# Kernel optimization log

Measured on AMD Instinct MI355X. Metric: run time of the kernel, lower is better.

Reference implementation:

```python
import jax, jax.numpy as jnp
import numpy as np

C = 1.0  # Poincare ball curvature
EPS = 1e-15


def setup_inputs() -> dict:
    key = jax.random.key(0)
    k1, k2, k3 = jax.random.split(key, 3)
    B, S, D_IN, D_OUT = 16, 8192, 128, 128
    # points strictly inside the unit ball: ||x|| ~ 0.05*sqrt(128) ~ 0.57
    x = 0.05 * jax.random.normal(k1, (B, S, D_IN), dtype=jnp.float32)
    z = 0.01 * jax.random.normal(k2, (D_IN, D_OUT), dtype=jnp.float32)  # init_std=0.01 normal
    r = 0.01 * jax.random.normal(k3, (D_OUT,), dtype=jnp.float32)
    return {"x": x, "z": z, "r": r}


def reference(x, z, r):
    # Poincare MLR (Shimizu et al., Hyperbolic NN++), as in hypll PoincareBall.mlr
    c = jnp.asarray(C, x.dtype)
    cs = jnp.sqrt(c)
    prefix = x.shape[:-1]
    x2 = x.reshape(-1, x.shape[-1])                       # [N, d_in]
    # conformal factor lambda_x = 2 / (1 - c ||x||^2)
    lam = 2.0 / (1.0 - c * jnp.sum(x2 * x2, axis=-1, keepdims=True))  # [N, 1]
    z_norm = jnp.maximum(jnp.linalg.norm(z, axis=0), EPS)             # [d_out]
    two_csr = 2.0 * cs * r                                            # [d_out]
    inner = x2 @ z                                                    # [N, d_out]
    arg = (cs * lam * inner / z_norm) * jnp.cosh(two_csr) - (lam - 1.0) * jnp.sinh(two_csr)
    out = (2.0 * z_norm / cs) * jnp.arcsinh(arg)                      # [N, d_out]
    return out.reshape(*prefix, z.shape[1])
```

## Files before the change

kernel.cpp:

```cpp
#include <hip/hip_runtime.h>
#include <cstdint>


typedef __attribute__((ext_vector_type(8))) short short8;
typedef __attribute__((ext_vector_type(4))) float floatx4;

#define D 128
#define ZT_STRIDE 136
#define TILE_M 128

__device__ inline unsigned bf16_rne(float f) {
    unsigned u = __float_as_uint(f);
    return ((u + 0x7FFFu + ((u >> 16) & 1u)) >> 16) & 0xFFFFu;
}

__global__ void hmlr_prep(const float* __restrict__ z, const float* __restrict__ r,
                          unsigned short* __restrict__ zt, float* __restrict__ An,
                          float* __restrict__ Bn, float* __restrict__ Sn) {
    int n = blockIdx.x;
    int k = threadIdx.x;
    float v = z[k * D + n];
    zt[n * ZT_STRIDE + k] = (unsigned short)bf16_rne(v);
    float p = v * v;
    #pragma unroll
    for (int off = 32; off >= 1; off >>= 1) p += __shfl_down(p, off, 64);
    __shared__ float tmp[2];
    if ((k & 63) == 0) tmp[k >> 6] = p;
    __syncthreads();
    if (k == 0) {
        float ss = tmp[0] + tmp[1];
        float zn = fmaxf(sqrtf(ss), 1e-15f);
        float tc = 2.0f * r[n];
        An[n] = coshf(tc) / zn;
        Bn[n] = sinhf(tc);
        Sn[n] = 2.0f * zn;
    }
}

__global__ __launch_bounds__(256) void hmlr_main(const float* __restrict__ x,
                                                 const unsigned short* __restrict__ zt,
                                                 const float* __restrict__ An,
                                                 const float* __restrict__ Bn,
                                                 const float* __restrict__ Sn,
                                                 float* __restrict__ out) {
    __shared__ __align__(16) unsigned short Xlds[TILE_M * ZT_STRIDE];
    __shared__ float rowss[TILE_M];

    const int t    = threadIdx.x;
    const int w    = t >> 6;
    const int l    = t & 63;
    const int quad = l >> 4;
    const int l15  = l & 15;

    const int row0 = blockIdx.x * TILE_M;
    const float4* xv = reinterpret_cast<const float4*>(x) + (size_t)blockIdx.x * (TILE_M * D / 4);

    #pragma unroll
    for (int i = 0; i < 16; ++i) {
        int f4  = t + 256 * i;
        float4 v = xv[f4];
        int row = f4 >> 5;
        int k4  = (f4 & 31) << 2;
        float ssq = v.x * v.x + v.y * v.y + v.z * v.z + v.w * v.w;
        ssq += __shfl_xor(ssq, 1);
        ssq += __shfl_xor(ssq, 2);
        ssq += __shfl_xor(ssq, 4);
        ssq += __shfl_xor(ssq, 8);
        ssq += __shfl_xor(ssq, 16);
        if ((t & 31) == 0) rowss[row] = ssq;
        unsigned lo = bf16_rne(v.x) | (bf16_rne(v.y) << 16);
        unsigned hi = bf16_rne(v.z) | (bf16_rne(v.w) << 16);
        *reinterpret_cast<uint2*>(&Xlds[row * ZT_STRIDE + k4]) = make_uint2(lo, hi);
    }
    __syncthreads();

    floatx4 acc[2][8];
    #pragma unroll
    for (int mt = 0; mt < 2; ++mt)
        #pragma unroll
        for (int nt = 0; nt < 8; ++nt)
            acc[mt][nt] = (floatx4){0.f, 0.f, 0.f, 0.f};

    #pragma unroll
    for (int kc = 0; kc < 4; ++kc) {
        const int kof = kc * 32 + quad * 8;
        short8 a0 = *reinterpret_cast<const short8*>(&Xlds[(w * 32 + l15) * ZT_STRIDE + kof]);
        short8 a1 = *reinterpret_cast<const short8*>(&Xlds[(w * 32 + 16 + l15) * ZT_STRIDE + kof]);
        #pragma unroll
        for (int nt = 0; nt < 8; ++nt) {
            short8 b = *reinterpret_cast<const short8*>(zt + (nt * 16 + l15) * ZT_STRIDE + kof);
            acc[0][nt] = __builtin_amdgcn_mfma_f32_16x16x32_bf16(a0, b, acc[0][nt], 0, 0, 0);
            acc[1][nt] = __builtin_amdgcn_mfma_f32_16x16x32_bf16(a1, b, acc[1][nt], 0, 0, 0);
        }
    }

    float anv[8], bnv[8], snv[8];
    #pragma unroll
    for (int nt = 0; nt < 8; ++nt) {
        int n = nt * 16 + l15;
        anv[nt] = An[n];
        bnv[nt] = Bn[n];
        snv[nt] = Sn[n];
    }
    #pragma unroll
    for (int mt = 0; mt < 2; ++mt) {
        #pragma unroll
        for (int reg = 0; reg < 4; ++reg) {
            int rlocal = w * 32 + mt * 16 + quad * 4 + reg;
            float lam  = 2.0f / (1.0f - rowss[rlocal]);
            float lm1  = lam - 1.0f;
            float* orow = out + (size_t)(row0 + rlocal) * D + l15;
            #pragma unroll
            for (int nt = 0; nt < 8; ++nt) {
                float inner = acc[mt][nt][reg];
                float arg = __fmaf_rn(lam * inner, anv[nt], -lm1 * bnv[nt]);
                float a  = fabsf(arg);
                float as = __logf(a + __fsqrt_rn(__fmaf_rn(a, a, 1.0f)));
                orow[nt * 16] = copysignf(as, arg) * snv[nt];
            }
        }
    }
}

extern "C" void kernel_launch(void* const* d_in, const int* in_sizes, int n_in,
                              void* d_out, int out_size, void* d_ws, size_t ws_size,
                              hipStream_t stream) {
    const float* x = (const float*)d_in[0];
    const float* z = (const float*)d_in[1];
    const float* r = (const float*)d_in[2];
    float* out = (float*)d_out;

    char* wsb = (char*)d_ws;
    unsigned short* zt = (unsigned short*)wsb;
    float* An = (float*)(wsb + 128 * ZT_STRIDE * sizeof(unsigned short));
    float* Bn = An + 128;
    float* Sn = An + 256;

    hmlr_prep<<<128, 128, 0, stream>>>(z, r, zt, An, Bn, Sn);

    const int n_rows = in_sizes[0] / D;
    hmlr_main<<<n_rows / TILE_M, 256, 0, stream>>>(x, zt, An, Bn, Sn, out);
}
```

Before: 147.8 us.

## Load x directly into MFMA A-fragments in registers, dropping LDS staging

Each lane now loads its own row's fp32 slice of x straight from global memory in the layout the MFMA A operand expects, converts it to bf16 in registers, and computes the row norm with cross-lane shuffles. This removes the LDS tile, the barrier and the LDS round trip. Block tile size drops to 64 rows, with each wave handling 16 rows, so there are twice as many blocks. The trade-off is less coalesced global loads (32-byte chunks per lane spread across rows) and a zt B-fragment reload per 16 rows instead of per 32.

Measured after the change: 140.3 us. 5.1% less time.

```diff
diff --git a/kernel.cpp b/kernel.cpp
--- a/kernel.cpp
+++ b/kernel.cpp
@@ -7,7 +7,6 @@
 
 #define D 128
 #define ZT_STRIDE 136
-#define TILE_M 128
 
 __device__ inline unsigned bf16_rne(float f) {
     unsigned u = __float_as_uint(f);
@@ -43,54 +42,57 @@
                                                  const float* __restrict__ Bn,
                                                  const float* __restrict__ Sn,
                                                  float* __restrict__ out) {
-    __shared__ __align__(16) unsigned short Xlds[TILE_M * ZT_STRIDE];
-    __shared__ float rowss[TILE_M];
-
     const int t    = threadIdx.x;
     const int w    = t >> 6;
     const int l    = t & 63;
     const int quad = l >> 4;
     const int l15  = l & 15;
 
-    const int row0 = blockIdx.x * TILE_M;
-    const float4* xv = reinterpret_cast<const float4*>(x) + (size_t)blockIdx.x * (TILE_M * D / 4);
+    const int rowbase = blockIdx.x * 64 + w * 16;
+    const int myrow   = rowbase + l15;
 
+    const float* xrow = x + (size_t)myrow * D + quad * 8;
+    float4 xv[8];
     #pragma unroll
-    for (int i = 0; i < 16; ++i) {
-        int f4  = t + 256 * i;
-        float4 v = xv[f4];
-        int row = f4 >> 5;
-        int k4  = (f4 & 31) << 2;
-        float ssq = v.x * v.x + v.y * v.y + v.z * v.z + v.w * v.w;
-        ssq += __shfl_xor(ssq, 1);
-        ssq += __shfl_xor(ssq, 2);
-        ssq += __shfl_xor(ssq, 4);
-        ssq += __shfl_xor(ssq, 8);
-        ssq += __shfl_xor(ssq, 16);
-        if ((t & 31) == 0) rowss[row] = ssq;
-        unsigned lo = bf16_rne(v.x) | (bf16_rne(v.y) << 16);
-        unsigned hi = bf16_rne(v.z) | (bf16_rne(v.w) << 16);
-        *reinterpret_cast<uint2*>(&Xlds[row * ZT_STRIDE + k4]) = make_uint2(lo, hi);
+    for (int kc = 0; kc < 4; ++kc) {
+        xv[2 * kc]     = *reinterpret_cast<const float4*>(xrow + kc * 32);
+        xv[2 * kc + 1] = *reinterpret_cast<const float4*>(xrow + kc * 32 + 4);
     }
-    __syncthreads();
 
-    floatx4 acc[2][8];
+    float ssq = 0.f;
     #pragma unroll
-    for (int mt = 0; mt < 2; ++mt)
-        #pragma unroll
-        for (int nt = 0; nt < 8; ++nt)
-            acc[mt][nt] = (floatx4){0.f, 0.f, 0.f, 0.f};
+    for (int i = 0; i < 8; ++i)
+        ssq += xv[i].x * xv[i].x + xv[i].y * xv[i].y + xv[i].z * xv[i].z + xv[i].w * xv[i].w;
+    ssq += __shfl_xor(ssq, 16);
+    ssq += __shfl_xor(ssq, 32);
+
+    short8 afrag[4];
+    #pragma unroll
+    for (int kc = 0; kc < 4; ++kc) {
+        float4 v0 = xv[2 * kc], v1 = xv[2 * kc + 1];
+        union { short8 s8; unsigned short u[8]; } af;
+        af.u[0] = (unsigned short)bf16_rne(v0.x);
+        af.u[1] = (unsigned short)bf16_rne(v0.y);
+        af.u[2] = (unsigned short)bf16_rne(v0.z);
+        af.u[3] = (unsigned short)bf16_rne(v0.w);
+        af.u[4] = (unsigned short)bf16_rne(v1.x);
+        af.u[5] = (unsigned short)bf16_rne(v1.y);
+        af.u[6] = (unsigned short)bf16_rne(v1.z);
+        af.u[7] = (unsigned short)bf16_rne(v1.w);
+        afrag[kc] = af.s8;
+    }
+
+    floatx4 acc[8];
+    #pragma unroll
+    for (int nt = 0; nt < 8; ++nt) acc[nt] = (floatx4){0.f, 0.f, 0.f, 0.f};
 
     #pragma unroll
     for (int kc = 0; kc < 4; ++kc) {
-        const int kof = kc * 32 + quad * 8;
-        short8 a0 = *reinterpret_cast<const short8*>(&Xlds[(w * 32 + l15) * ZT_STRIDE + kof]);
-        short8 a1 = *reinterpret_cast<const short8*>(&Xlds[(w * 32 + 16 + l15) * ZT_STRIDE + kof]);
+        const unsigned short* zb = zt + kc * 32 + quad * 8;
         #pragma unroll
         for (int nt = 0; nt < 8; ++nt) {
-            short8 b = *reinterpret_cast<const short8*>(zt + (nt * 16 + l15) * ZT_STRIDE + kof);
-            acc[0][nt] = __builtin_amdgcn_mfma_f32_16x16x32_bf16(a0, b, acc[0][nt], 0, 0, 0);
-            acc[1][nt] = __builtin_amdgcn_mfma_f32_16x16x32_bf16(a1, b, acc[1][nt], 0, 0, 0);
+            short8 b = *reinterpret_cast<const short8*>(zb + (nt * 16 + l15) * ZT_STRIDE);
+            acc[nt] = __builtin_amdgcn_mfma_f32_16x16x32_bf16(afrag[kc], b, acc[nt], 0, 0, 0);
         }
     }
 
@@ -103,21 +105,18 @@
         snv[nt] = Sn[n];
     }
     #pragma unroll
-    for (int mt = 0; mt < 2; ++mt) {
+    for (int reg = 0; reg < 4; ++reg) {
+        float rss = __shfl(ssq, quad * 4 + reg);
+        float lam = 2.0f / (1.0f - rss);
+        float lm1 = lam - 1.0f;
+        float* orow = out + (size_t)(rowbase + quad * 4 + reg) * D + l15;
         #pragma unroll
-        for (int reg = 0; reg < 4; ++reg) {
-            int rlocal = w * 32 + mt * 16 + quad * 4 + reg;
-            float lam  = 2.0f / (1.0f - rowss[rlocal]);
-            float lm1  = lam - 1.0f;
-            float* orow = out + (size_t)(row0 + rlocal) * D + l15;
-            #pragma unroll
-            for (int nt = 0; nt < 8; ++nt) {
-                float inner = acc[mt][nt][reg];
-                float arg = __fmaf_rn(lam * inner, anv[nt], -lm1 * bnv[nt]);
-                float a  = fabsf(arg);
-                float as = __logf(a + __fsqrt_rn(__fmaf_rn(a, a, 1.0f)));
-                orow[nt * 16] = copysignf(as, arg) * snv[nt];
-            }
+        for (int nt = 0; nt < 8; ++nt) {
+            float inner = acc[nt][reg];
+            float arg = __fmaf_rn(lam * inner, anv[nt], -lm1 * bnv[nt]);
+            float a   = fabsf(arg);
+            float as  = __logf(a + __fsqrt_rn(__fmaf_rn(a, a, 1.0f)));
+            orow[nt * 16] = copysignf(as, arg) * snv[nt];
         }
     }
 }
@@ -139,5 +138,5 @@
     hmlr_prep<<<128, 128, 0, stream>>>(z, r, zt, An, Bn, Sn);
 
     const int n_rows = in_sizes[0] / D;
-    hmlr_main<<<n_rows / TILE_M, 256, 0, stream>>>(x, zt, An, Bn, Sn, out);
+    hmlr_main<<<n_rows / 64, 256, 0, stream>>>(x, zt, An, Bn, Sn, out);
 }
```
